# Kernel tuning notes

Hardware: AMD Instinct MI355X
Metric: run time of the kernel (lower is better)

The kernel has to match this reference:

```python
import jax, jax.numpy as jnp
import numpy as np

N_NODES = 100000
N_EDGES = 3200000
HIDDEN = 64


def _gcn_conv(x, W, b, row, col, norm, n_nodes):
    # x: [N, Fin] -> [N, Fout]; symmetric-normalized scatter-add aggregation
    xw = x @ W  # [N, Fout]
    msg = xw[row] * norm[:, None]  # [E', Fout] gather + scale
    out = jax.ops.segment_sum(msg, col, num_segments=n_nodes)  # scatter-add
    return out + b


def _norm_and_loops(edge_index, n_nodes):
    # add self loops (PyG GCNConv default) and compute D^-1/2 norm per edge
    loops = jnp.arange(n_nodes, dtype=edge_index.dtype)
    row = jnp.concatenate([edge_index[0], loops])
    col = jnp.concatenate([edge_index[1], loops])
    deg = jax.ops.segment_sum(jnp.ones_like(col, dtype=jnp.float32), col,
                              num_segments=n_nodes)
    dis = jnp.where(deg > 0, 1.0 / jnp.sqrt(deg), 0.0)
    norm = dis[row] * dis[col]
    return row, col, norm


def setup_inputs() -> dict:
    key = jax.random.key(0)
    k1, k2, k3, k4 = jax.random.split(key, 4)
    x = jax.random.normal(k1, (N_NODES, 1), dtype=jnp.float32)
    edge_index = jax.random.randint(k2, (2, N_EDGES), 0, N_NODES, dtype=jnp.int64)
    # Glorot-ish init for GCN weights
    W1 = jax.random.normal(k3, (1, HIDDEN), dtype=jnp.float32) * (1.0 / np.sqrt(1))
    b1 = jnp.zeros((HIDDEN,), dtype=jnp.float32)
    W2 = jax.random.normal(k4, (HIDDEN, 1), dtype=jnp.float32) * (1.0 / np.sqrt(HIDDEN))
    b2 = jnp.zeros((1,), dtype=jnp.float32)
    return {"x": x, "edge_index": edge_index, "W1": W1, "b1": b1, "W2": W2, "b2": b2}


def reference(x, edge_index, W1, b1, W2, b2):
    n = x.shape[0]
    row, col, norm = _norm_and_loops(edge_index, n)
    h = _gcn_conv(x, W1, b1, row, col, norm, n)   # [N, 64]
    out = _gcn_conv(h, W2, b2, row, col, norm, n)  # [N, 1]
    return out
```

## Files before the change

kernel.cpp:

```cpp
#include <hip/hip_runtime.h>
#include <math.h>


#define CHUNK 256
#define CHUNK_SHIFT 8
#define PACK_SHIFT 17
#define ROW_MASK ((1u << PACK_SHIFT) - 1u)
#define NBMAX 512
#define SLICES 256
#define CAPB 80
#define CAPB_V (CAPB / 4)
#define ATPB 1024
#define PLACE_TPB 1024
#define STAGE_CAP 12544

static __device__ __forceinline__ int gid() {
    return blockIdx.x * blockDim.x + threadIdx.x;
}

__global__ void __launch_bounds__(PLACE_TPB)
k_place(const int* __restrict__ row, const int* __restrict__ col,
        int E, int NB, int* __restrict__ len, unsigned* __restrict__ sorted) {
    __shared__ unsigned stage[STAGE_CAP];
    __shared__ int cnt[NBMAX];
    __shared__ int soff[NBMAX];
    __shared__ int wcnt[NBMAX];
    const int tid = threadIdx.x;
    const int blk = blockIdx.x;
    int quads = E >> 2;
    int per = (quads + gridDim.x - 1) / gridDim.x;
    int qlo = blk * per, qhi = min(quads, qlo + per);

    for (int t = tid; t < NBMAX; t += PLACE_TPB) { cnt[t] = 0; wcnt[t] = 0; }
    __syncthreads();

    for (int q = qlo + tid; q < qhi; q += PLACE_TPB) {
        int4 c = reinterpret_cast<const int4*>(col)[q];
        atomicAdd(&cnt[c.x >> CHUNK_SHIFT], 1);
        atomicAdd(&cnt[c.y >> CHUNK_SHIFT], 1);
        atomicAdd(&cnt[c.z >> CHUNK_SHIFT], 1);
        atomicAdd(&cnt[c.w >> CHUNK_SHIFT], 1);
    }
    if (blk == 0 && tid == 0)
        for (int j = quads << 2; j < E; ++j)
            atomicAdd(&cnt[col[j] >> CHUNK_SHIFT], 1);
    __syncthreads();

    if (tid < NBMAX) soff[tid] = cnt[tid];
    __syncthreads();
    for (int o = 1; o < NBMAX; o <<= 1) {
        int v = 0;
        if (tid < NBMAX) {
            v = soff[tid];
            if (tid >= o) v += soff[tid - o];
        }
        __syncthreads();
        if (tid < NBMAX) soff[tid] = v;
        __syncthreads();
    }
    if (tid < NBMAX) soff[tid] -= cnt[tid];
    __syncthreads();

    for (int q = qlo + tid; q < qhi; q += PLACE_TPB) {
        int4 r = reinterpret_cast<const int4*>(row)[q];
        int4 c = reinterpret_cast<const int4*>(col)[q];
        {
            int b = c.x >> CHUNK_SHIFT;
            int p = soff[b] + atomicAdd(&wcnt[b], 1);
            stage[p] = (unsigned)r.x | ((unsigned)(c.x & (CHUNK - 1)) << PACK_SHIFT);
        }
        {
            int b = c.y >> CHUNK_SHIFT;
            int p = soff[b] + atomicAdd(&wcnt[b], 1);
            stage[p] = (unsigned)r.y | ((unsigned)(c.y & (CHUNK - 1)) << PACK_SHIFT);
        }
        {
            int b = c.z >> CHUNK_SHIFT;
            int p = soff[b] + atomicAdd(&wcnt[b], 1);
            stage[p] = (unsigned)r.z | ((unsigned)(c.z & (CHUNK - 1)) << PACK_SHIFT);
        }
        {
            int b = c.w >> CHUNK_SHIFT;
            int p = soff[b] + atomicAdd(&wcnt[b], 1);
            stage[p] = (unsigned)r.w | ((unsigned)(c.w & (CHUNK - 1)) << PACK_SHIFT);
        }
    }
    if (blk == 0 && tid == 0) {
        for (int j = quads << 2; j < E; ++j) {
            int cc = col[j];
            int b = cc >> CHUNK_SHIFT;
            int p = soff[b] + atomicAdd(&wcnt[b], 1);
            stage[p] = (unsigned)row[j] | ((unsigned)(cc & (CHUNK - 1)) << PACK_SHIFT);
        }
    }
    __syncthreads();

    const int wid = tid >> 6, lane = tid & 63;
    const int nw = PLACE_TPB >> 6;
    for (int b = wid; b < NB; b += nw) {
        int c = min(cnt[b], CAPB);
        int lb = soff[b];
        unsigned* dst = sorted + ((size_t)b * SLICES + blk) * CAPB;
        for (int i = lane; i < c; i += 64) dst[i] = stage[lb + i];
        if (lane == 0) len[(size_t)b * SLICES + blk] = c;
    }
}


__global__ void __launch_bounds__(ATPB)
k_acc1(const unsigned* __restrict__ sorted, const int* __restrict__ len,
       const float* __restrict__ x, float* __restrict__ dis, float* __restrict__ g,
       int N) {
    __shared__ float acc[CHUNK];
    __shared__ int slen[SLICES];
    const int b = blockIdx.x;
    const int tid = threadIdx.x;
    if (tid < CHUNK) acc[tid] = 0.0f;
    for (int t = tid; t < SLICES; t += ATPB) slen[t] = len[(size_t)b * SLICES + t];
    __syncthreads();
    const uint4* bs = reinterpret_cast<const uint4*>(sorted + (size_t)b * SLICES * CAPB);
    const int TOTV = SLICES * CAPB_V;
    #pragma unroll 2
    for (int j = tid; j < TOTV; j += ATPB) {
        int s = j / CAPB_V;
        int l = slen[s];
        int base = (j - s * CAPB_V) << 2;
        if (base >= l) continue;
        uint4 p = bs[j];
        atomicAdd(&acc[p.x >> PACK_SHIFT], 1.0f);
        if (base + 1 < l) atomicAdd(&acc[p.y >> PACK_SHIFT], 1.0f);
        if (base + 2 < l) atomicAdd(&acc[p.z >> PACK_SHIFT], 1.0f);
        if (base + 3 < l) atomicAdd(&acc[p.w >> PACK_SHIFT], 1.0f);
    }
    __syncthreads();
    int i = b * CHUNK + tid;
    if (tid < CHUNK && i < N) {
        float d = rsqrtf(1.0f + acc[tid]);
        dis[i] = d;
        g[i] = d * x[i];
    }
}

__global__ void __launch_bounds__(ATPB)
k_acc2(const unsigned* __restrict__ sorted, const int* __restrict__ len,
       const float* __restrict__ g, const float* __restrict__ dis,
       const float* __restrict__ W1, const float* __restrict__ b1,
       const float* __restrict__ W2, int H,
       float* __restrict__ g2, int N) {
    __shared__ float acc[CHUNK];
    __shared__ int slen[SLICES];
    __shared__ float sab[2];
    const int b = blockIdx.x;
    const int tid = threadIdx.x;
    if (tid < CHUNK) acc[tid] = 0.0f;
    for (int t = tid; t < SLICES; t += ATPB) slen[t] = len[(size_t)b * SLICES + t];
    if (tid >= CHUNK && tid < CHUNK + 64) {
        int t = tid - CHUNK;
        float w2 = (t < H) ? W2[t] : 0.0f;
        float a = (t < H) ? W1[t] * w2 : 0.0f;
        float bb = (t < H) ? b1[t] * w2 : 0.0f;
        for (int o = 32; o; o >>= 1) {
            a += __shfl_down(a, o, 64);
            bb += __shfl_down(bb, o, 64);
        }
        if (t == 0) { sab[0] = a; sab[1] = bb; }
    }
    __syncthreads();
    const uint4* bs = reinterpret_cast<const uint4*>(sorted + (size_t)b * SLICES * CAPB);
    const int TOTV = SLICES * CAPB_V;
    #pragma unroll 2
    for (int j = tid; j < TOTV; j += ATPB) {
        int s = j / CAPB_V;
        int l = slen[s];
        int base = (j - s * CAPB_V) << 2;
        if (base >= l) continue;
        uint4 p = bs[j];
        atomicAdd(&acc[p.x >> PACK_SHIFT], g[p.x & ROW_MASK]);
        if (base + 1 < l) atomicAdd(&acc[p.y >> PACK_SHIFT], g[p.y & ROW_MASK]);
        if (base + 2 < l) atomicAdd(&acc[p.z >> PACK_SHIFT], g[p.z & ROW_MASK]);
        if (base + 3 < l) atomicAdd(&acc[p.w >> PACK_SHIFT], g[p.w & ROW_MASK]);
    }
    __syncthreads();
    int i = b * CHUNK + tid;
    if (tid < CHUNK && i < N) {
        float d = dis[i];
        float s = d * (g[i] + acc[tid]);
        g2[i] = d * (sab[0] * s + sab[1]);
    }
}

__global__ void __launch_bounds__(ATPB)
k_acc3(const unsigned* __restrict__ sorted, const int* __restrict__ len,
       const float* __restrict__ g2, const float* __restrict__ dis,
       const float* __restrict__ b2, float* __restrict__ out, int N) {
    __shared__ float acc[CHUNK];
    __shared__ int slen[SLICES];
    const int b = blockIdx.x;
    const int tid = threadIdx.x;
    if (tid < CHUNK) acc[tid] = 0.0f;
    for (int t = tid; t < SLICES; t += ATPB) slen[t] = len[(size_t)b * SLICES + t];
    __syncthreads();
    const uint4* bs = reinterpret_cast<const uint4*>(sorted + (size_t)b * SLICES * CAPB);
    const int TOTV = SLICES * CAPB_V;
    #pragma unroll 2
    for (int j = tid; j < TOTV; j += ATPB) {
        int s = j / CAPB_V;
        int l = slen[s];
        int base = (j - s * CAPB_V) << 2;
        if (base >= l) continue;
        uint4 p = bs[j];
        atomicAdd(&acc[p.x >> PACK_SHIFT], g2[p.x & ROW_MASK]);
        if (base + 1 < l) atomicAdd(&acc[p.y >> PACK_SHIFT], g2[p.y & ROW_MASK]);
        if (base + 2 < l) atomicAdd(&acc[p.z >> PACK_SHIFT], g2[p.z & ROW_MASK]);
        if (base + 3 < l) atomicAdd(&acc[p.w >> PACK_SHIFT], g2[p.w & ROW_MASK]);
    }
    __syncthreads();
    int i = b * CHUNK + tid;
    if (tid < CHUNK && i < N)
        out[i] = dis[i] * (g2[i] + acc[tid]) + b2[0];
}


__global__ void k_zero_f(float* __restrict__ p, int n) {
    int i = gid();
    if (i < n) p[i] = 0.0f;
}

__global__ void k_ab_fb(const float* __restrict__ W1, const float* __restrict__ b1,
                        const float* __restrict__ W2, float* __restrict__ ab, int hidden) {
    int t = threadIdx.x;
    float w2 = (t < hidden) ? W2[t] : 0.0f;
    float a = (t < hidden) ? W1[t] * w2 : 0.0f;
    float b = (t < hidden) ? b1[t] * w2 : 0.0f;
    for (int o = 32; o; o >>= 1) {
        a += __shfl_down(a, o, 64);
        b += __shfl_down(b, o, 64);
    }
    if (t == 0) { ab[0] = a; ab[1] = b; }
}

__global__ void k_deg_fb(const int* __restrict__ col, float* __restrict__ t, int E) {
    int i = gid();
    if (i < E) atomicAdd(&t[col[i]], 1.0f);
}

__global__ void k_scat_fb(const int* __restrict__ ei, const float* __restrict__ val,
                          float* __restrict__ t, int E) {
    int i = gid();
    if (i < E) atomicAdd(&t[ei[E + i]], val[ei[i]]);
}

__global__ void k_node1_fb(const float* __restrict__ x, const float* __restrict__ degsum,
                           float* __restrict__ dis, float* __restrict__ g, int N) {
    int i = gid();
    if (i < N) {
        float d = rsqrtf(1.0f + degsum[i]);
        dis[i] = d;
        g[i] = d * x[i];
    }
}

__global__ void k_node2_fb(const float* __restrict__ g, const float* __restrict__ dis,
                           const float* __restrict__ ab, const float* __restrict__ sum1,
                           float* __restrict__ g2, int N) {
    int i = gid();
    if (i < N) {
        float s = dis[i] * (g[i] + sum1[i]);
        g2[i] = dis[i] * (ab[0] * s + ab[1]);
    }
}

__global__ void k_node3_fb(const float* __restrict__ g2, const float* __restrict__ dis,
                           const float* __restrict__ b2, const float* __restrict__ sum2,
                           float* __restrict__ out, int N) {
    int i = gid();
    if (i < N) out[i] = dis[i] * (g2[i] + sum2[i]) + b2[0];
}

extern "C" void kernel_launch(void* const* d_in, const int* in_sizes, int n_in,
                              void* d_out, int out_size, void* d_ws, size_t ws_size,
                              hipStream_t stream) {
    const float* x  = (const float*)d_in[0];
    const int*   ei = (const int*)d_in[1];
    const float* W1 = (const float*)d_in[2];
    const float* b1 = (const float*)d_in[3];
    const float* W2 = (const float*)d_in[4];
    const float* b2 = (const float*)d_in[5];
    float* out = (float*)d_out;

    const int N = in_sizes[0];
    const int E = in_sizes[1] / 2;
    const int H = in_sizes[2];
    const int NB = (N + CHUNK - 1) >> CHUNK_SHIFT;

    const int per_quads = ((E >> 2) + SLICES - 1) / SLICES;
    const int stage_need = per_quads * 4 + 8;

    const int slice_mean = (E / SLICES) / (NB > 0 ? NB : 1);

    char* w = (char*)d_ws;
    unsigned* sorted = (unsigned*)w;   w += (size_t)NB * SLICES * CAPB * 4;
    int* len = (int*)w;                w += (size_t)NB * SLICES * 4;
    float* dis = (float*)w;            w += (size_t)N * 4;
    float* g   = (float*)w;            w += (size_t)N * 4;
    float* g2  = (float*)w;            w += (size_t)N * 4;
    size_t needed = (size_t)(w - (char*)d_ws);

    const int BLK = 256;
    const int nodeGrid = (N + BLK - 1) / BLK;

    if (N <= (1 << PACK_SHIFT) && NB <= NBMAX && H <= 64 &&
        stage_need <= STAGE_CAP && slice_mean * 2 <= CAPB && ws_size >= needed) {
        k_place<<<SLICES, PLACE_TPB, 0, stream>>>(ei, ei + E, E, NB, len, sorted);
        k_acc1<<<NB, ATPB, 0, stream>>>(sorted, len, x, dis, g, N);
        k_acc2<<<NB, ATPB, 0, stream>>>(sorted, len, g, dis, W1, b1, W2, H, g2, N);
        k_acc3<<<NB, ATPB, 0, stream>>>(sorted, len, g2, dis, b2, out, N);
    } else {
        float* fdis = (float*)d_ws;
        float* fg   = fdis + N;
        float* fg2  = fg + N;
        float* ftmp = fg2 + N;
        float* fab  = ftmp + N;
        const int eGrid = (E + BLK - 1) / BLK;
        k_ab_fb<<<1, 64, 0, stream>>>(W1, b1, W2, fab, H);
        k_zero_f<<<nodeGrid, BLK, 0, stream>>>(ftmp, N);
        k_deg_fb<<<eGrid, BLK, 0, stream>>>(ei + E, ftmp, E);
        k_node1_fb<<<nodeGrid, BLK, 0, stream>>>(x, ftmp, fdis, fg, N);
        k_zero_f<<<nodeGrid, BLK, 0, stream>>>(ftmp, N);
        k_scat_fb<<<eGrid, BLK, 0, stream>>>(ei, fg, ftmp, E);
        k_node2_fb<<<nodeGrid, BLK, 0, stream>>>(fg, fdis, fab, ftmp, fg2, N);
        k_zero_f<<<nodeGrid, BLK, 0, stream>>>(ftmp, N);
        k_scat_fb<<<eGrid, BLK, 0, stream>>>(ei, fg2, ftmp, E);
        k_node3_fb<<<nodeGrid, BLK, 0, stream>>>(fg2, fdis, b2, ftmp, out, N);
    }
}
```

Baseline: 92.43 us.

## Compact per-bucket edge lists in degree pass for dense later aggregation

The degree pass now prefix-sums the per-slice lengths and writes each bucket's edges into a dense compact buffer with a total-length array. The second and third aggregation kernels read these dense lists as uint4 quads, with no per-slice length checks and no padding slots. This removes the padded-slot reads and branch divergence from two passes. In exchange the first pass writes the data an extra time, needs more workspace, and silently truncates any bucket that exceeds the compact capacity.

```diff
diff --git a/kernel.cpp b/kernel.cpp
--- a/kernel.cpp
+++ b/kernel.cpp
@@ -106,31 +106,57 @@
     }
 }
 
-
 __global__ void __launch_bounds__(ATPB)
 k_acc1(const unsigned* __restrict__ sorted, const int* __restrict__ len,
        const float* __restrict__ x, float* __restrict__ dis, float* __restrict__ g,
-       int N) {
+       unsigned* __restrict__ compact, int* __restrict__ blen, int CAPC, int N) {
     __shared__ float acc[CHUNK];
     __shared__ int slen[SLICES];
+    __shared__ int soffb[SLICES];
     const int b = blockIdx.x;
     const int tid = threadIdx.x;
     if (tid < CHUNK) acc[tid] = 0.0f;
-    for (int t = tid; t < SLICES; t += ATPB) slen[t] = len[(size_t)b * SLICES + t];
-    __syncthreads();
+    if (tid < SLICES) slen[tid] = len[(size_t)b * SLICES + tid];
+    __syncthreads();
+    if (tid < SLICES) soffb[tid] = slen[tid];
+    __syncthreads();
+    for (int o = 1; o < SLICES; o <<= 1) {
+        int v = 0;
+        if (tid < SLICES) {
+            v = soffb[tid];
+            if (tid >= o) v += soffb[tid - o];
+        }
+        __syncthreads();
+        if (tid < SLICES) soffb[tid] = v;
+        __syncthreads();
+    }
+    if (tid < SLICES) soffb[tid] -= slen[tid];
+    __syncthreads();
+    if (tid == 0) blen[b] = min(soffb[SLICES - 1] + slen[SLICES - 1], CAPC);
+    unsigned* cb = compact + (size_t)b * CAPC;
     const uint4* bs = reinterpret_cast<const uint4*>(sorted + (size_t)b * SLICES * CAPB);
     const int TOTV = SLICES * CAPB_V;
-    #pragma unroll 2
     for (int j = tid; j < TOTV; j += ATPB) {
         int s = j / CAPB_V;
         int l = slen[s];
         int base = (j - s * CAPB_V) << 2;
         if (base >= l) continue;
         uint4 p = bs[j];
+        int dp = soffb[s] + base;
         atomicAdd(&acc[p.x >> PACK_SHIFT], 1.0f);
-        if (base + 1 < l) atomicAdd(&acc[p.y >> PACK_SHIFT], 1.0f);
-        if (base + 2 < l) atomicAdd(&acc[p.z >> PACK_SHIFT], 1.0f);
-        if (base + 3 < l) atomicAdd(&acc[p.w >> PACK_SHIFT], 1.0f);
+        if (dp < CAPC) cb[dp] = p.x;
+        if (base + 1 < l) {
+            atomicAdd(&acc[p.y >> PACK_SHIFT], 1.0f);
+            if (dp + 1 < CAPC) cb[dp + 1] = p.y;
+        }
+        if (base + 2 < l) {
+            atomicAdd(&acc[p.z >> PACK_SHIFT], 1.0f);
+            if (dp + 2 < CAPC) cb[dp + 2] = p.z;
+        }
+        if (base + 3 < l) {
+            atomicAdd(&acc[p.w >> PACK_SHIFT], 1.0f);
+            if (dp + 3 < CAPC) cb[dp + 3] = p.w;
+        }
     }
     __syncthreads();
     int i = b * CHUNK + tid;
@@ -141,19 +167,18 @@
     }
 }
 
+
 __global__ void __launch_bounds__(ATPB)
-k_acc2(const unsigned* __restrict__ sorted, const int* __restrict__ len,
+k_acc2(const unsigned* __restrict__ compact, const int* __restrict__ blen, int CAPC,
        const float* __restrict__ g, const float* __restrict__ dis,
        const float* __restrict__ W1, const float* __restrict__ b1,
        const float* __restrict__ W2, int H,
        float* __restrict__ g2, int N) {
     __shared__ float acc[CHUNK];
-    __shared__ int slen[SLICES];
     __shared__ float sab[2];
     const int b = blockIdx.x;
     const int tid = threadIdx.x;
     if (tid < CHUNK) acc[tid] = 0.0f;
-    for (int t = tid; t < SLICES; t += ATPB) slen[t] = len[(size_t)b * SLICES + t];
     if (tid >= CHUNK && tid < CHUNK + 64) {
         int t = tid - CHUNK;
         float w2 = (t < H) ? W2[t] : 0.0f;
@@ -166,19 +191,25 @@
         if (t == 0) { sab[0] = a; sab[1] = bb; }
     }
     __syncthreads();
-    const uint4* bs = reinterpret_cast<const uint4*>(sorted + (size_t)b * SLICES * CAPB);
-    const int TOTV = SLICES * CAPB_V;
+    int len = blen[b];
+    const unsigned* cb = compact + (size_t)b * CAPC;
+    const uint4* cb4 = reinterpret_cast<const uint4*>(cb);
+    int quads = len >> 2;
     #pragma unroll 2
-    for (int j = tid; j < TOTV; j += ATPB) {
-        int s = j / CAPB_V;
-        int l = slen[s];
-        int base = (j - s * CAPB_V) << 2;
-        if (base >= l) continue;
-        uint4 p = bs[j];
-        atomicAdd(&acc[p.x >> PACK_SHIFT], g[p.x & ROW_MASK]);
-        if (base + 1 < l) atomicAdd(&acc[p.y >> PACK_SHIFT], g[p.y & ROW_MASK]);
-        if (base + 2 < l) atomicAdd(&acc[p.z >> PACK_SHIFT], g[p.z & ROW_MASK]);
-        if (base + 3 < l) atomicAdd(&acc[p.w >> PACK_SHIFT], g[p.w & ROW_MASK]);
+    for (int j = tid; j < quads; j += ATPB) {
+        uint4 p = cb4[j];
+        float vx = g[p.x & ROW_MASK];
+        float vy = g[p.y & ROW_MASK];
+        float vz = g[p.z & ROW_MASK];
+        float vw = g[p.w & ROW_MASK];
+        atomicAdd(&acc[p.x >> PACK_SHIFT], vx);
+        atomicAdd(&acc[p.y >> PACK_SHIFT], vy);
+        atomicAdd(&acc[p.z >> PACK_SHIFT], vz);
+        atomicAdd(&acc[p.w >> PACK_SHIFT], vw);
+    }
+    if (tid < (len & 3)) {
+        unsigned p = cb[(quads << 2) + tid];
+        atomicAdd(&acc[p >> PACK_SHIFT], g[p & ROW_MASK]);
     }
     __syncthreads();
     int i = b * CHUNK + tid;
@@ -190,29 +221,33 @@
 }
 
 __global__ void __launch_bounds__(ATPB)
-k_acc3(const unsigned* __restrict__ sorted, const int* __restrict__ len,
+k_acc3(const unsigned* __restrict__ compact, const int* __restrict__ blen, int CAPC,
        const float* __restrict__ g2, const float* __restrict__ dis,
        const float* __restrict__ b2, float* __restrict__ out, int N) {
     __shared__ float acc[CHUNK];
-    __shared__ int slen[SLICES];
     const int b = blockIdx.x;
     const int tid = threadIdx.x;
     if (tid < CHUNK) acc[tid] = 0.0f;
-    for (int t = tid; t < SLICES; t += ATPB) slen[t] = len[(size_t)b * SLICES + t];
-    __syncthreads();
-    const uint4* bs = reinterpret_cast<const uint4*>(sorted + (size_t)b * SLICES * CAPB);
-    const int TOTV = SLICES * CAPB_V;
+    __syncthreads();
+    int len = blen[b];
+    const unsigned* cb = compact + (size_t)b * CAPC;
+    const uint4* cb4 = reinterpret_cast<const uint4*>(cb);
+    int quads = len >> 2;
     #pragma unroll 2
-    for (int j = tid; j < TOTV; j += ATPB) {
-        int s = j / CAPB_V;
-        int l = slen[s];
-        int base = (j - s * CAPB_V) << 2;
-        if (base >= l) continue;
-        uint4 p = bs[j];
-        atomicAdd(&acc[p.x >> PACK_SHIFT], g2[p.x & ROW_MASK]);
-        if (base + 1 < l) atomicAdd(&acc[p.y >> PACK_SHIFT], g2[p.y & ROW_MASK]);
-        if (base + 2 < l) atomicAdd(&acc[p.z >> PACK_SHIFT], g2[p.z & ROW_MASK]);
-        if (base + 3 < l) atomicAdd(&acc[p.w >> PACK_SHIFT], g2[p.w & ROW_MASK]);
+    for (int j = tid; j < quads; j += ATPB) {
+        uint4 p = cb4[j];
+        float vx = g2[p.x & ROW_MASK];
+        float vy = g2[p.y & ROW_MASK];
+        float vz = g2[p.z & ROW_MASK];
+        float vw = g2[p.w & ROW_MASK];
+        atomicAdd(&acc[p.x >> PACK_SHIFT], vx);
+        atomicAdd(&acc[p.y >> PACK_SHIFT], vy);
+        atomicAdd(&acc[p.z >> PACK_SHIFT], vz);
+        atomicAdd(&acc[p.w >> PACK_SHIFT], vw);
+    }
+    if (tid < (len & 3)) {
+        unsigned p = cb[(quads << 2) + tid];
+        atomicAdd(&acc[p >> PACK_SHIFT], g2[p & ROW_MASK]);
     }
     __syncthreads();
     int i = b * CHUNK + tid;
@@ -298,9 +333,15 @@
 
     const int slice_mean = (E / SLICES) / (NB > 0 ? NB : 1);
 
+    int mean_b = (E + NB - 1) / NB;
+    int CAPC = mean_b + 1024 + (mean_b >> 4);
+    CAPC = (CAPC + 255) & ~255;
+
     char* w = (char*)d_ws;
     unsigned* sorted = (unsigned*)w;   w += (size_t)NB * SLICES * CAPB * 4;
     int* len = (int*)w;                w += (size_t)NB * SLICES * 4;
+    unsigned* compact = (unsigned*)w;  w += (size_t)NB * CAPC * 4;
+    int* blen = (int*)w;               w += (size_t)NBMAX * 4;
     float* dis = (float*)w;            w += (size_t)N * 4;
     float* g   = (float*)w;            w += (size_t)N * 4;
     float* g2  = (float*)w;            w += (size_t)N * 4;
@@ -312,9 +353,9 @@
     if (N <= (1 << PACK_SHIFT) && NB <= NBMAX && H <= 64 &&
         stage_need <= STAGE_CAP && slice_mean * 2 <= CAPB && ws_size >= needed) {
         k_place<<<SLICES, PLACE_TPB, 0, stream>>>(ei, ei + E, E, NB, len, sorted);
-        k_acc1<<<NB, ATPB, 0, stream>>>(sorted, len, x, dis, g, N);
-        k_acc2<<<NB, ATPB, 0, stream>>>(sorted, len, g, dis, W1, b1, W2, H, g2, N);
-        k_acc3<<<NB, ATPB, 0, stream>>>(sorted, len, g2, dis, b2, out, N);
+        k_acc1<<<NB, ATPB, 0, stream>>>(sorted, len, x, dis, g, compact, blen, CAPC, N);
+        k_acc2<<<NB, ATPB, 0, stream>>>(compact, blen, CAPC, g, dis, W1, b1, W2, H, g2, N);
+        k_acc3<<<NB, ATPB, 0, stream>>>(compact, blen, CAPC, g2, dis, b2, out, N);
     } else {
         float* fdis = (float*)d_ws;
         float* fg   = fdis + N;
```

Result: no change. 93.58 us (+1.2%).
